# Performance work log

Measured on AMD Instinct MI355X. Metric: run time of the kernel, lower is better.

## Reference

```python
import jax, jax.numpy as jnp
import numpy as np

B = 2_097_152          # batch of theta samples
POLY_DEG = 127         # QSP polynomial degree -> 128 phases
PI = np.float32(np.pi)


def setup_inputs() -> dict:
    key = jax.random.key(0)
    k1, k2 = jax.random.split(key)
    th = jax.random.uniform(k1, (B, 1), dtype=jnp.float32) * PI
    phis = jax.random.uniform(k2, (POLY_DEG + 1, 1), dtype=jnp.float32) * PI
    return {"th": th, "phis": phis}


def reference(th, phis):
    # th: [B,1] float32, phis: [P+1,1] float32 (learned QSP phases)
    theta = th[:, 0]                      # [B]
    c = jnp.cos(theta)
    s = jnp.sin(theta)
    # expm(i*theta*X) = cos(theta) I + i sin(theta) X  (closed form, no expm)
    wx = jnp.stack(
        [jnp.stack([c + 0j, 1j * s], axis=-1),
         jnp.stack([1j * s, c + 0j], axis=-1)],
        axis=-2,
    ).astype(jnp.complex64)               # [B,2,2]

    phi = phis[:, 0]                      # [P+1]
    e = jnp.exp(1j * phi).astype(jnp.complex64)
    # expm(i*phi*Z) = diag(e^{i phi}, e^{-i phi})
    rz = (jnp.zeros((phi.shape[0], 2, 2), jnp.complex64)
          .at[:, 0, 0].set(e)
          .at[:, 1, 1].set(jnp.conj(e)))  # [P+1,2,2]

    u0 = jnp.broadcast_to(rz[0], (theta.shape[0], 2, 2))  # [B,2,2]

    def step(u, rzk):
        u = jnp.einsum('bij,bjk->bik', u, wx)   # u @ W(x)
        u = jnp.einsum('bij,jk->bik', u, rzk)   # ... @ Rz(phi_k)
        return u, None

    u, _ = jax.lax.scan(step, u0, rz[1:])       # 127 sequential steps
    # convention == 0: (Re[u_00], Im[u_00])
    return (jnp.real(u[:, 0, 0]), jnp.imag(u[:, 0, 0]))
```

## Files before the change

### kernel.cpp

```cpp
#include <hip/hip_runtime.h>


#define NPHI 128

__device__ __forceinline__ float wave_shr1(float x) {
    return __builtin_bit_cast(float,
        __builtin_amdgcn_update_dpp(0, __builtin_bit_cast(int, x),
                                    0x138, 0xf, 0xf, true));
}

__global__ __launch_bounds__(64) void qsp_gamma(const float* __restrict__ phis,
                                                float4* __restrict__ gout)
{
    __shared__ float2 h[NPHI];
    const int L = threadIdx.x;

    float sp, cp;
    __sincosf(phis[L], &sp, &cp);
    h[L] = make_float2(0.5f * cp, 0.5f * sp);
    __sincosf(phis[L + 64], &sp, &cp);
    h[L + 64] = make_float2(0.5f * cp, 0.5f * sp);

    float A0r = 0.f, A0i = 0.f, B0r = 0.f, B0i = 0.f;
    float A1r = 0.f, A1i = 0.f, B1r = 0.f, B1i = 0.f;
    const float2 h0 = h[0];
    if (L == 0) { A0r = 2.f * h0.x; A0i = 2.f * h0.y; }

    #pragma unroll 4
    for (int k = 1; k < NPHI; ++k) {
        const float2 hk = h[k];
        const float hx = hk.x, hy = hk.y;
        const float pAr = wave_shr1(A1r), pAi = wave_shr1(A1i);
        const float pBr = wave_shr1(B1r), pBi = wave_shr1(B1i);
        const float u0r = pAr + pBr, u0i = pAi + pBi;
        const float v0r = A0r - B0r, v0i = A0i - B0i;
        const float sA0r = u0r + v0r, sA0i = u0i + v0i;
        const float sB0r = u0r - v0r, sB0i = u0i - v0i;
        const float u1r = A0r + B0r, u1i = A0i + B0i;
        const float v1r = A1r - B1r, v1i = A1i - B1i;
        const float sA1r = u1r + v1r, sA1i = u1i + v1i;
        const float sB1r = u1r - v1r, sB1i = u1i - v1i;
        A0r = fmaf(hx, sA0r, -hy * sA0i);
        A0i = fmaf(hx, sA0i,  hy * sA0r);
        B0r = fmaf(hx, sB0r,  hy * sB0i);
        B0i = fmaf(hx, sB0i, -hy * sB0r);
        A1r = fmaf(hx, sA1r, -hy * sA1i);
        A1i = fmaf(hx, sA1i,  hy * sA1r);
        B1r = fmaf(hx, sB1r,  hy * sB1i);
        B1i = fmaf(hx, sB1i, -hy * sB1r);
    }
    gout[L] = make_float4(A0r, A0i, A1r, A1i);
}

__global__ __launch_bounds__(256, 4) void qsp_main(
    const float* __restrict__ th,
    const float4* __restrict__ g4,
    float* __restrict__ out,
    int Bq8)
{
    const int tid = threadIdx.x;
    const int idx = blockIdx.x * blockDim.x + tid;
    const int lidx = (idx < Bq8) ? idx : 0;
    const float4 ta = ((const float4*)th)[2 * lidx];
    const float4 tb = ((const float4*)th)[2 * lidx + 1];
    const float th8[8] = {ta.x, ta.y, ta.z, ta.w, tb.x, tb.y, tb.z, tb.w};

    float zr[8], zi[8];
    #pragma unroll
    for (int e = 0; e < 8; ++e) {
        float s, c;
        __sincosf(2.f * th8[e], &s, &c);
        zr[e] = c; zi[e] = s;
    }

    float ar[8], ai[8];
    #pragma unroll
    for (int e = 0; e < 8; ++e) { ar[e] = 0.f; ai[e] = 0.f; }

    float4 gA = g4[62];
    float4 gB = g4[63];

    #define QSP_STEP(gr, gi)                                                  \
        _Pragma("unroll")                                                     \
        for (int e = 0; e < 8; ++e) {                                         \
            const float nr = fmaf(ar[e], zr[e], fmaf(-ai[e], zi[e], (gr)));   \
            const float ni = fmaf(ar[e], zi[e], fmaf( ai[e], zr[e], (gi)));   \
            ar[e] = nr; ai[e] = ni;                                           \
        }

    #pragma unroll 1
    for (int jj = 62; jj >= 2; jj -= 2) {
        const float4 nA = g4[jj - 2];
        const float4 nB = g4[jj - 1];
        __builtin_amdgcn_sched_barrier(0);
        QSP_STEP(gB.z, gB.w)
        QSP_STEP(gB.x, gB.y)
        QSP_STEP(gA.z, gA.w)
        QSP_STEP(gA.x, gA.y)
        gA = nA; gB = nB;
    }
    QSP_STEP(gB.z, gB.w)
    QSP_STEP(gB.x, gB.y)
    QSP_STEP(gA.z, gA.w)
    QSP_STEP(gA.x, gA.y)
    #undef QSP_STEP

    float orv[8], oiv[8];
    #pragma unroll
    for (int e = 0; e < 8; ++e) {
        float S, C;
        __sincosf(127.f * th8[e], &S, &C);
        orv[e] = fmaf(ar[e], C,  ai[e] * S);
        oiv[e] = fmaf(ai[e], C, -ar[e] * S);
    }

    if (idx < Bq8) {
        float4* o4 = (float4*)out;
        const int ib = 2 * Bq8;
        o4[2 * idx]          = make_float4(orv[0], orv[1], orv[2], orv[3]);
        o4[2 * idx + 1]      = make_float4(orv[4], orv[5], orv[6], orv[7]);
        o4[ib + 2 * idx]     = make_float4(oiv[0], oiv[1], oiv[2], oiv[3]);
        o4[ib + 2 * idx + 1] = make_float4(oiv[4], oiv[5], oiv[6], oiv[7]);
    }
}

extern "C" void kernel_launch(void* const* d_in, const int* in_sizes, int n_in,
                              void* d_out, int out_size, void* d_ws, size_t ws_size,
                              hipStream_t stream)
{
    const float* th   = (const float*)d_in[0];
    const float* phis = (const float*)d_in[1];
    float* out = (float*)d_out;
    const int B = in_sizes[0];
    const int Bq8 = B >> 3;
    const int block = 256;
    const int grid = (Bq8 + block - 1) / block;

    float4* gbuf = (float4*)d_ws;

    qsp_gamma<<<1, 64, 0, stream>>>(phis, gbuf);
    qsp_main<<<grid, block, 0, stream>>>(th, gbuf, out, Bq8);
}
```

Measured before the change: 89.18 us.

## Fuse gamma coefficient recurrence into main kernel using per-wave readlane broadcasts

```diff
diff --git a/kernel.cpp b/kernel.cpp
--- a/kernel.cpp
+++ b/kernel.cpp
@@ -1,7 +1,5 @@
 #include <hip/hip_runtime.h>
 
-
-#define NPHI 128
 
 __device__ __forceinline__ float wave_shr1(float x) {
     return __builtin_bit_cast(float,
@@ -9,62 +7,66 @@
                                     0x138, 0xf, 0xf, true));
 }
 
-__global__ __launch_bounds__(64) void qsp_gamma(const float* __restrict__ phis,
-                                                float4* __restrict__ gout)
+__device__ __forceinline__ float rlane(float x, int l) {
+    return __builtin_bit_cast(float,
+        __builtin_amdgcn_readlane(__builtin_bit_cast(int, x), l));
+}
+
+__global__ __launch_bounds__(256, 4) void qsp_fused(
+    const float* __restrict__ th,
+    const float* __restrict__ phis,
+    float* __restrict__ out,
+    int Bq8)
 {
-    __shared__ float2 h[NPHI];
-    const int L = threadIdx.x;
+    const int tid  = threadIdx.x;
+    const int lane = tid & 63;
+    const int idx  = blockIdx.x * blockDim.x + tid;
+    const int lidx = (idx < Bq8) ? idx : 0;
+
+    const float4 ta = ((const float4*)th)[2 * lidx];
+    const float4 tb = ((const float4*)th)[2 * lidx + 1];
 
     float sp, cp;
-    __sincosf(phis[L], &sp, &cp);
-    h[L] = make_float2(0.5f * cp, 0.5f * sp);
-    __sincosf(phis[L + 64], &sp, &cp);
-    h[L + 64] = make_float2(0.5f * cp, 0.5f * sp);
+    __sincosf(phis[lane], &sp, &cp);
+    const float hAx = 0.5f * cp, hAy = 0.5f * sp;
+    __sincosf(phis[lane + 64], &sp, &cp);
+    const float hBx = 0.5f * cp, hBy = 0.5f * sp;
 
     float A0r = 0.f, A0i = 0.f, B0r = 0.f, B0i = 0.f;
     float A1r = 0.f, A1i = 0.f, B1r = 0.f, B1i = 0.f;
-    const float2 h0 = h[0];
-    if (L == 0) { A0r = 2.f * h0.x; A0i = 2.f * h0.y; }
+    const float h0x = rlane(hAx, 0), h0y = rlane(hAy, 0);
+    if (lane == 0) { A0r = 2.f * h0x; A0i = 2.f * h0y; }
+
+    #define QSP_REC(hx_, hy_)                                                 \
+    {                                                                         \
+        const float hx = (hx_), hy = (hy_);                                   \
+        const float pAr = wave_shr1(A1r), pAi = wave_shr1(A1i);               \
+        const float pBr = wave_shr1(B1r), pBi = wave_shr1(B1i);               \
+        const float u0r = pAr + pBr, u0i = pAi + pBi;                         \
+        const float v0r = A0r - B0r, v0i = A0i - B0i;                         \
+        const float sA0r = u0r + v0r, sA0i = u0i + v0i;                       \
+        const float sB0r = u0r - v0r, sB0i = u0i - v0i;                       \
+        const float u1r = A0r + B0r, u1i = A0i + B0i;                         \
+        const float v1r = A1r - B1r, v1i = A1i - B1i;                         \
+        const float sA1r = u1r + v1r, sA1i = u1i + v1i;                       \
+        const float sB1r = u1r - v1r, sB1i = u1i - v1i;                       \
+        A0r = fmaf(hx, sA0r, -hy * sA0i);                                     \
+        A0i = fmaf(hx, sA0i,  hy * sA0r);                                     \
+        B0r = fmaf(hx, sB0r,  hy * sB0i);                                     \
+        B0i = fmaf(hx, sB0i, -hy * sB0r);                                     \
+        A1r = fmaf(hx, sA1r, -hy * sA1i);                                     \
+        A1i = fmaf(hx, sA1i,  hy * sA1r);                                     \
+        B1r = fmaf(hx, sB1r,  hy * sB1i);                                     \
+        B1i = fmaf(hx, sB1i, -hy * sB1r);                                     \
+    }
 
     #pragma unroll 4
-    for (int k = 1; k < NPHI; ++k) {
-        const float2 hk = h[k];
-        const float hx = hk.x, hy = hk.y;
-        const float pAr = wave_shr1(A1r), pAi = wave_shr1(A1i);
-        const float pBr = wave_shr1(B1r), pBi = wave_shr1(B1i);
-        const float u0r = pAr + pBr, u0i = pAi + pBi;
-        const float v0r = A0r - B0r, v0i = A0i - B0i;
-        const float sA0r = u0r + v0r, sA0i = u0i + v0i;
-        const float sB0r = u0r - v0r, sB0i = u0i - v0i;
-        const float u1r = A0r + B0r, u1i = A0i + B0i;
-        const float v1r = A1r - B1r, v1i = A1i - B1i;
-        const float sA1r = u1r + v1r, sA1i = u1i + v1i;
-        const float sB1r = u1r - v1r, sB1i = u1i - v1i;
-        A0r = fmaf(hx, sA0r, -hy * sA0i);
-        A0i = fmaf(hx, sA0i,  hy * sA0r);
-        B0r = fmaf(hx, sB0r,  hy * sB0i);
-        B0i = fmaf(hx, sB0i, -hy * sB0r);
-        A1r = fmaf(hx, sA1r, -hy * sA1i);
-        A1i = fmaf(hx, sA1i,  hy * sA1r);
-        B1r = fmaf(hx, sB1r,  hy * sB1i);
-        B1i = fmaf(hx, sB1i, -hy * sB1r);
-    }
-    gout[L] = make_float4(A0r, A0i, A1r, A1i);
-}
+    for (int k = 1; k < 64; ++k)   QSP_REC(rlane(hAx, k), rlane(hAy, k))
+    #pragma unroll 4
+    for (int k = 0; k < 64; ++k)   QSP_REC(rlane(hBx, k), rlane(hBy, k))
+    #undef QSP_REC
 
-__global__ __launch_bounds__(256, 4) void qsp_main(
-    const float* __restrict__ th,
-    const float4* __restrict__ g4,
-    float* __restrict__ out,
-    int Bq8)
-{
-    const int tid = threadIdx.x;
-    const int idx = blockIdx.x * blockDim.x + tid;
-    const int lidx = (idx < Bq8) ? idx : 0;
-    const float4 ta = ((const float4*)th)[2 * lidx];
-    const float4 tb = ((const float4*)th)[2 * lidx + 1];
     const float th8[8] = {ta.x, ta.y, ta.z, ta.w, tb.x, tb.y, tb.z, tb.w};
-
     float zr[8], zi[8];
     #pragma unroll
     for (int e = 0; e < 8; ++e) {
@@ -77,9 +79,6 @@
     #pragma unroll
     for (int e = 0; e < 8; ++e) { ar[e] = 0.f; ai[e] = 0.f; }
 
-    float4 gA = g4[62];
-    float4 gB = g4[63];
-
     #define QSP_STEP(gr, gi)                                                  \
         _Pragma("unroll")                                                     \
         for (int e = 0; e < 8; ++e) {                                         \
@@ -88,21 +87,13 @@
             ar[e] = nr; ai[e] = ni;                                           \
         }
 
-    #pragma unroll 1
-    for (int jj = 62; jj >= 2; jj -= 2) {
-        const float4 nA = g4[jj - 2];
-        const float4 nB = g4[jj - 1];
-        __builtin_amdgcn_sched_barrier(0);
-        QSP_STEP(gB.z, gB.w)
-        QSP_STEP(gB.x, gB.y)
-        QSP_STEP(gA.z, gA.w)
-        QSP_STEP(gA.x, gA.y)
-        gA = nA; gB = nB;
+    #pragma unroll 2
+    for (int jj = 63; jj >= 0; --jj) {
+        const float g1r = rlane(A1r, jj), g1i = rlane(A1i, jj);
+        QSP_STEP(g1r, g1i)
+        const float g0r = rlane(A0r, jj), g0i = rlane(A0i, jj);
+        QSP_STEP(g0r, g0i)
     }
-    QSP_STEP(gB.z, gB.w)
-    QSP_STEP(gB.x, gB.y)
-    QSP_STEP(gA.z, gA.w)
-    QSP_STEP(gA.x, gA.y)
     #undef QSP_STEP
 
     float orv[8], oiv[8];
@@ -135,9 +126,5 @@
     const int Bq8 = B >> 3;
     const int block = 256;
     const int grid = (Bq8 + block - 1) / block;
-
-    float4* gbuf = (float4*)d_ws;
-
-    qsp_gamma<<<1, 64, 0, stream>>>(phis, gbuf);
-    qsp_main<<<grid, block, 0, stream>>>(th, gbuf, out, Bq8);
+    qsp_fused<<<grid, block, 0, stream>>>(th, phis, out, Bq8);
 }
```

Measured after the change: 103.1 us. +15.6%, slower.
